# Optimization experiments

Measured on AMD Instinct MI355X. Metric: run time of the kernel, lower is better.

## Reference

```python
import jax, jax.numpy as jnp
import numpy as np

N_NODES = 100000
N_HEDGES = 200000
N_INC = 1000000
N_GRAPHS = 256
H = 64        # h_dim
HE = 35       # hedge_fea_dim
HOUT = 128    # hout_dim
NL = 3        # n_layers
EPS = 1e-5


def _segment_mean(vals, idx, num_segments):
    s = jax.ops.segment_sum(vals, idx, num_segments=num_segments)
    cnt = jax.ops.segment_sum(jnp.ones((vals.shape[0],), vals.dtype), idx,
                              num_segments=num_segments)
    return s / jnp.maximum(cnt, 1.0)[:, None]


def _bn(z, g, b):
    # training-mode BatchNorm1d: batch stats, biased variance
    m = jnp.mean(z, axis=0)
    v = jnp.var(z, axis=0)
    return (z - m) * jax.lax.rsqrt(v + EPS) * g + b


def setup_inputs() -> dict:
    key = jax.random.key(0)
    ks = jax.random.split(key, 32)
    inp = {
        "x": jax.random.normal(ks[0], (N_NODES, 92), jnp.float32),
        "node_idx": jax.random.randint(ks[1], (N_INC,), 0, N_NODES),
        "hedge_idx": jax.random.randint(ks[2], (N_INC,), 0, N_HEDGES),
        "hedge_attr": jax.random.normal(ks[3], (N_HEDGES, HE), jnp.float32),
        "batch": jnp.sort(jax.random.randint(ks[4], (N_NODES,), 0, N_GRAPHS)),
    }
    s = 0.05
    cat = H + HE  # 99
    inp["embed_w"] = jax.random.normal(ks[5], (92, H), jnp.float32) * s
    inp["embed_b"] = jnp.zeros((H,), jnp.float32)
    inp["f1_w"] = jax.random.normal(ks[6], (NL, cat, HE), jnp.float32) * s
    inp["f1_b"] = jnp.zeros((NL, HE), jnp.float32)
    inp["c1_w"] = jax.random.normal(ks[7], (NL, cat, HE), jnp.float32) * s
    inp["c1_b"] = jnp.zeros((NL, HE), jnp.float32)
    inp["f2_w"] = jax.random.normal(ks[8], (NL, cat, H), jnp.float32) * s
    inp["f2_b"] = jnp.zeros((NL, H), jnp.float32)
    inp["c2_w"] = jax.random.normal(ks[9], (NL, cat, H), jnp.float32) * s
    inp["c2_b"] = jnp.zeros((NL, H), jnp.float32)
    inp["bnf_g"] = jnp.ones((NL, HE), jnp.float32)
    inp["bnf_b"] = jnp.zeros((NL, HE), jnp.float32)
    inp["bnc_g"] = jnp.ones((NL, HE), jnp.float32)
    inp["bnc_b"] = jnp.zeros((NL, HE), jnp.float32)
    inp["bno_g"] = jnp.ones((NL, H), jnp.float32)
    inp["bno_b"] = jnp.zeros((NL, H), jnp.float32)
    inp["l2_w"] = jax.random.normal(ks[10], (H, HOUT), jnp.float32) * s
    inp["l2_b"] = jnp.zeros((HOUT,), jnp.float32)
    inp["out_w"] = jax.random.normal(ks[11], (HOUT, 1), jnp.float32) * s
    inp["out_b"] = jnp.zeros((1,), jnp.float32)
    return inp


def reference(x, node_idx, hedge_idx, hedge_attr, batch,
              embed_w, embed_b, f1_w, f1_b, c1_w, c1_b,
              f2_w, f2_b, c2_w, c2_b,
              bnf_g, bnf_b, bnc_g, bnc_b, bno_g, bno_b,
              l2_w, l2_b, out_w, out_b):
    sp = jax.nn.softplus
    x = x @ embed_w + embed_b  # [N, H]
    for i in range(NL):
        # gather node feats per incidence, mean over each hyperedge
        hx = _segment_mean(x[node_idx], hedge_idx, N_HEDGES)       # [NH, H]
        msg = jnp.concatenate([hx, hedge_attr], axis=1)            # [NH, H+HE]
        z_f = _bn(msg @ f1_w[i] + f1_b[i], bnf_g[i], bnf_b[i])
        z_c = _bn(msg @ c1_w[i] + c1_b[i], bnc_g[i], bnc_b[i])
        hedge_attr = jax.nn.sigmoid(z_f) * sp(z_c)                 # [NH, HE]
        z = jnp.concatenate([x[node_idx], hedge_attr[hedge_idx]], axis=-1)  # [E, H+HE]
        o = jax.nn.sigmoid(z @ f2_w[i] + f2_b[i]) * sp(z @ c2_w[i] + c2_b[i])  # [E, H]
        o = _segment_mean(o, node_idx, N_NODES)                    # [N, H]
        o = _bn(o, bno_g[i], bno_b[i])
        x = sp(o + x)
    pooled = _segment_mean(x, batch, N_GRAPHS)                     # [G, H]
    h = sp(pooled @ l2_w + l2_b)                                   # [G, HOUT]
    return h @ out_w + out_b                                       # [G, 1]
```

## Files before the change

kernel.cpp:

```cpp
#include <hip/hip_runtime.h>
#include <math.h>

#define N_NODES 100000
#define N_HEDGES 200000
#define N_INC 1000000
#define N_GRAPHS 256
#define HD 64
#define HE 35
#define CAT 99
#define EPSB 1e-5f

typedef __attribute__((ext_vector_type(8))) short short8;
typedef __attribute__((ext_vector_type(4))) float f32x4;

__device__ __forceinline__ float sp_f(float x) {
  return fmaxf(x, 0.f) + __logf(1.f + __expf(-fabsf(x)));
}
__device__ __forceinline__ float sig_f(float x) {
  return __builtin_amdgcn_rcpf(1.f + __expf(-x));
}
__device__ __forceinline__ unsigned bfr(float x) {
  unsigned u = __float_as_uint(x);
  return (u + 0x7fffu + ((u >> 16) & 1u)) >> 16;
}
__device__ __forceinline__ unsigned pk2(float lo, float hi) {
  return bfr(lo) | (bfr(hi) << 16);
}
__device__ __forceinline__ float blo(unsigned v) { return __uint_as_float(v << 16); }
__device__ __forceinline__ float bhi(unsigned v) {
  return __uint_as_float(v & 0xffff0000u);
}
__device__ __forceinline__ float bf2f(unsigned short s) {
  return __uint_as_float(((unsigned)s) << 16);
}

__global__ __launch_bounds__(256) void k_hist(const int* __restrict__ nidx,
                                              const int* __restrict__ hidx,
                                              int* __restrict__ degN,
                                              int* __restrict__ degH,
                                              int* __restrict__ rankN,
                                              int* __restrict__ rankH) {
  int e = blockIdx.x * 256 + threadIdx.x;
  if (e >= N_INC) return;
  rankH[e] = atomicAdd(&degH[hidx[e]], 1);
  rankN[e] = atomicAdd(&degN[nidx[e]], 1);
}

#define CHB ((N_HEDGES + 255) / 256)
#define CNB ((N_NODES + 255) / 256)

__global__ __launch_bounds__(256) void k_bsum(const int* __restrict__ degH,
                                              const int* __restrict__ degN,
                                              int* __restrict__ bsum) {
  __shared__ int s[256];
  int b = blockIdx.x, t = threadIdx.x;
  const int* deg;
  int n, i;
  if (b < CHB) {
    deg = degH; n = N_HEDGES; i = b * 256 + t;
  } else {
    deg = degN; n = N_NODES; i = (b - CHB) * 256 + t;
  }
  s[t] = (i < n) ? deg[i] : 0;
  __syncthreads();
  for (int st = 128; st > 0; st >>= 1) {
    if (t < st) s[t] += s[t + st];
    __syncthreads();
  }
  if (t == 0) bsum[b] = s[0];
}

__global__ __launch_bounds__(64) void k_bscan(int* __restrict__ bsum) {
  int seg0 = (blockIdx.x == 0) ? 0 : CHB;
  int segn = (blockIdx.x == 0) ? CHB : CNB;
  int lane = threadIdx.x;
  int carry = 0;
  for (int base = 0; base < segn; base += 64) {
    int i = base + lane;
    int orig = (i < segn) ? bsum[seg0 + i] : 0;
    int v = orig;
    for (int st = 1; st < 64; st <<= 1) {
      int u = __shfl_up(v, st);
      if (lane >= st) v += u;
    }
    int total = __shfl(v, 63);
    if (i < segn) bsum[seg0 + i] = carry + (v - orig);
    carry += total;
  }
}

__global__ __launch_bounds__(256) void k_alloc2(const int* __restrict__ degH,
                                                const int* __restrict__ degN,
                                                const int* __restrict__ bsum,
                                                int* __restrict__ offH,
                                                int* __restrict__ offN,
                                                float* __restrict__ invdH) {
  __shared__ int s[256];
  int b = blockIdx.x, t = threadIdx.x;
  const int* deg;
  int* off;
  int n, i;
  bool isH = (b < CHB);
  if (isH) {
    deg = degH; off = offH; n = N_HEDGES; i = b * 256 + t;
  } else {
    deg = degN; off = offN; n = N_NODES; i = (b - CHB) * 256 + t;
  }
  int d = (i < n) ? deg[i] : 0;
  s[t] = d;
  __syncthreads();
  for (int st = 1; st < 256; st <<= 1) {
    int u = 0;
    if (t >= st) u = s[t - st];
    __syncthreads();
    if (t >= st) s[t] += u;
    __syncthreads();
  }
  if (i < n) {
    off[i] = s[t] - d + bsum[b];
    if (isH) invdH[i] = 1.f / (float)max(d, 1);
  }
}

__global__ __launch_bounds__(256) void k_fill(const int* __restrict__ nidx,
                                              const int* __restrict__ hidx,
                                              const int* __restrict__ rankH,
                                              const int* __restrict__ rankN,
                                              const int* __restrict__ offH,
                                              const int* __restrict__ offN,
                                              int* __restrict__ permHn,
                                              int* __restrict__ permNh,
                                              int* __restrict__ offH_sent) {
  int e = blockIdx.x * 256 + threadIdx.x;
  if (e >= N_INC) return;
  if (e == 0) *offH_sent = N_INC;
  int nd = nidx[e], hg = hidx[e];
  permHn[offH[hg] + rankH[e]] = nd;
  permNh[offN[nd] + rankN[e]] = hg;
}

__global__ __launch_bounds__(64) void k_wpack(const float* __restrict__ f1w,
                                              const float* __restrict__ c1w,
                                              uint4* __restrict__ wpk) {
  int b = blockIdx.x;
  int layer = b / 20, rem = b % 20, ct = rem / 4, ks = rem % 4;
  int lane = threadIdx.x;
  int col = ct * 16 + (lane & 15);
  int k0 = ks * 32 + (lane >> 4) * 8;
  const float* wf = f1w + layer * CAT * HE;
  const float* wc = c1w + layer * CAT * HE;
  unsigned v[4];
#pragma unroll
  for (int p = 0; p < 4; ++p) {
    float lo = 0.f, hi = 0.f;
    int ka = k0 + p * 2, kb = ka + 1;
    if (ka < 99) {
      if (col < 35) lo = wf[ka * 35 + col];
      else if (col >= 36 && col < 71) lo = wc[ka * 35 + (col - 36)];
    }
    if (kb < 99) {
      if (col < 35) hi = wf[kb * 35 + col];
      else if (col >= 36 && col < 71) hi = wc[kb * 35 + (col - 36)];
    }
    v[p] = pk2(lo, hi);
  }
  uint4 o;
  o.x = v[0]; o.y = v[1]; o.z = v[2]; o.w = v[3];
  wpk[b * 64 + lane] = o;
}

__global__ __launch_bounds__(256) void k_cvt_ha(const float* __restrict__ src,
                                                unsigned short* __restrict__ dst,
                                                int n) {
  int t = blockIdx.x * 256 + threadIdx.x;
  if (t < n) dst[t] = (unsigned short)bfr(src[t]);
}

__global__ __launch_bounds__(256) void k_embed(const float* __restrict__ x,
                                               const float* __restrict__ w,
                                               const float* __restrict__ b,
                                               unsigned short* __restrict__ outb) {
  __shared__ float ws[92 * 64];
  __shared__ float rs[16][93];
  int tid = threadIdx.x;
  for (int i = tid; i < 92 * 64; i += 256) ws[i] = w[i];
  int r0 = blockIdx.x * 16;
  for (int i = tid; i < 16 * 92; i += 256) {
    int r = i / 92, k = i - r * 92;
    rs[r][k] = x[(r0 + r) * 92 + k];
  }
  __syncthreads();
  int h = tid & 63;
  float bias = b[h];
  for (int rr = tid >> 6; rr < 16; rr += 4) {
    float acc = bias;
    for (int k = 0; k < 92; ++k) acc += rs[rr][k] * ws[k * 64 + h];
    outb[(r0 + rr) * 64 + h] = (unsigned short)bfr(acc);
  }
}

#define GR 64
__global__ __launch_bounds__(256) void k_hedge_gemm(
    const unsigned short* __restrict__ xb, const int* __restrict__ permHn,
    const int* __restrict__ offH, const float* __restrict__ invdH,
    const unsigned short* __restrict__ hab, const uint4* __restrict__ wpk,
    unsigned short* __restrict__ z, float* __restrict__ stats) {
  __shared__ unsigned short msg[GR * 128];
  __shared__ float ps[160];
  __shared__ int bndL[4][18];
  int tid = threadIdx.x;
  int w = tid >> 6, lane = tid & 63;
  int r0 = blockIdx.x * GR;
  if (tid < 160) ps[tid] = 0.f;

  short8 bfg[5][4];
#pragma unroll
  for (int ct = 0; ct < 5; ++ct)
#pragma unroll
    for (int ks = 0; ks < 4; ++ks)
      bfg[ct][ks] = __builtin_bit_cast(short8, wpk[(ct * 4 + ks) * 64 + lane]);

  char* mb = (char*)msg;
  for (int i = tid; i < GR * 64; i += 256) {
    int r = i >> 6, c = 64 + (i & 63);
    unsigned short hv = 0;
    if (c < 99) hv = hab[(size_t)(r0 + r) * 35 + (c - 64)];
    *(unsigned short*)(mb + ((r * 256 + c * 2) ^ ((r & 7) << 4))) = hv;
  }

  int r0w = r0 + w * 16;
  if (lane < 17) bndL[w][lane] = offH[r0w + lane];
  int eBeg = bndL[w][0], eEnd = bndL[w][16];

  int j = 0;
  int nb = bndL[w][1];
  float acc = 0.f;
  for (int chunk = eBeg; chunk < eEnd; chunk += 8) {
    float v[8];
#pragma unroll
    for (int t = 0; t < 8; ++t) {
      int idx = permHn[min(chunk + t, eEnd - 1)];
      v[t] = bf2f(xb[(size_t)idx * 64 + lane]);
    }
#pragma unroll
    for (int t = 0; t < 8; ++t) {
      int e = chunk + t;
      if (e >= eEnd) break;
      while (e >= nb) {
        int rl = w * 16 + j;
        unsigned short mv = (unsigned short)bfr(acc * invdH[r0w + j]);
        *(unsigned short*)(mb + ((rl * 256 + lane * 2) ^ ((rl & 7) << 4))) = mv;
        acc = 0.f;
        ++j;
        nb = bndL[w][j + 1];
      }
      acc += v[t];
    }
  }
  for (; j < 16; ++j) {
    int rl = w * 16 + j;
    unsigned short mv = (unsigned short)bfr(acc * invdH[r0w + j]);
    *(unsigned short*)(mb + ((rl * 256 + lane * 2) ^ ((rl & 7) << 4))) = mv;
    acc = 0.f;
  }
  __syncthreads();

  {
    int rloc = w * 16 + (lane & 15);
    short8 a[4];
#pragma unroll
    for (int ks = 0; ks < 4; ++ks) {
      int byte = rloc * 256 + (ks * 32 + (lane >> 4) * 8) * 2;
      a[ks] = *(const short8*)(mb + (byte ^ ((rloc & 7) << 4)));
    }
#pragma unroll
    for (int ct = 0; ct < 5; ++ct) {
      f32x4 acc4 = {0.f, 0.f, 0.f, 0.f};
#pragma unroll
      for (int ks = 0; ks < 4; ++ks)
        acc4 = __builtin_amdgcn_mfma_f32_16x16x32_bf16(a[ks], bfg[ct][ks], acc4, 0, 0, 0);
      float s = (acc4[0] + acc4[1]) + (acc4[2] + acc4[3]);
      float q = (acc4[0] * acc4[0] + acc4[1] * acc4[1]) +
                (acc4[2] * acc4[2] + acc4[3] * acc4[3]);
      s += __shfl_xor(s, 16);
      s += __shfl_xor(s, 32);
      q += __shfl_xor(q, 16);
      q += __shfl_xor(q, 32);
      int col = ct * 16 + (lane & 15);
      if ((lane >> 4) == 0 && col < 72) {
        atomicAdd(&ps[col], s);
        atomicAdd(&ps[80 + col], q);
      }
      int growb = r0 + w * 16 + ((lane >> 4) << 2);
      if (col < 72) {
#pragma unroll
        for (int r = 0; r < 4; ++r)
          z[(size_t)(growb + r) * 72 + col] = (unsigned short)bfr(acc4[r]);
      }
    }
  }
  __syncthreads();
  if (tid < 160) atomicAdd(&stats[tid], ps[tid]);
}

__global__ __launch_bounds__(256) void k_hedge_post(
    const unsigned short* __restrict__ z, const float* __restrict__ stats,
    const float* __restrict__ gf, const float* __restrict__ bf_,
    const float* __restrict__ gc, const float* __restrict__ bc_,
    const float* __restrict__ f2wb, const float* __restrict__ c2wb,
    const float* __restrict__ f2b, const float* __restrict__ c2b,
    unsigned short* __restrict__ hab, unsigned* __restrict__ Vfc) {
  __shared__ float wf[35 * 64];
  __shared__ float wc[35 * 64];
  __shared__ float rs[16][36];
  __shared__ float sf[4][35];
  int tid = threadIdx.x;
  for (int i = tid; i < 35 * 64; i += 256) {
    wf[i] = f2wb[i];
    wc[i] = c2wb[i];
  }
  if (tid < 35) {
    const float inv = 1.f / N_HEDGES;
    float mf = stats[tid] * inv;
    float vf = stats[80 + tid] * inv - mf * mf;
    float mc = stats[36 + tid] * inv;
    float vc = stats[116 + tid] * inv - mc * mc;
    float a = rsqrtf(vf + EPSB) * gf[tid];
    float b = rsqrtf(vc + EPSB) * gc[tid];
    sf[0][tid] = a;
    sf[1][tid] = bf_[tid] - mf * a;
    sf[2][tid] = b;
    sf[3][tid] = bc_[tid] - mc * b;
  }
  __syncthreads();
  int r0 = blockIdx.x * 16;
  for (int i = tid; i < 16 * 35; i += 256) {
    int r = i / 35, c = i - r * 35;
    const unsigned short* zr = &z[(size_t)(r0 + r) * 72];
    float nf = bf2f(zr[c]) * sf[0][c] + sf[1][c];
    float nc = bf2f(zr[36 + c]) * sf[2][c] + sf[3][c];
    float ha = sig_f(nf) * sp_f(nc);
    rs[r][c] = ha;
    hab[(size_t)(r0 + r) * 35 + c] = (unsigned short)bfr(ha);
  }
  __syncthreads();
  int h = tid & 63, rb = tid >> 6;
  float af0, af1, af2, af3, ac0, ac1, ac2, ac3;
  af0 = af1 = af2 = af3 = f2b[h];
  ac0 = ac1 = ac2 = ac3 = c2b[h];
  for (int k = 0; k < 35; ++k) {
    float wfv = wf[k * 64 + h], wcv = wc[k * 64 + h];
    float m0 = rs[rb][k], m1 = rs[rb + 4][k], m2 = rs[rb + 8][k], m3 = rs[rb + 12][k];
    af0 += m0 * wfv; ac0 += m0 * wcv;
    af1 += m1 * wfv; ac1 += m1 * wcv;
    af2 += m2 * wfv; ac2 += m2 * wcv;
    af3 += m3 * wfv; ac3 += m3 * wcv;
  }
  int row = r0 + rb;
  Vfc[row * 64 + h] = pk2(af0, ac0);
  Vfc[(row + 4) * 64 + h] = pk2(af1, ac1);
  Vfc[(row + 8) * 64 + h] = pk2(af2, ac2);
  Vfc[(row + 12) * 64 + h] = pk2(af3, ac3);
}

__global__ __launch_bounds__(256) void k_uv_node(const unsigned short* __restrict__ xb,
                                                 const float* __restrict__ f2w,
                                                 const float* __restrict__ c2w,
                                                 unsigned* __restrict__ Ufc) {
  __shared__ float wf[64 * 64];
  __shared__ float wc[64 * 64];
  __shared__ float rs[16][65];
  int tid = threadIdx.x;
  for (int i = tid; i < 64 * 64; i += 256) {
    wf[i] = f2w[i];
    wc[i] = c2w[i];
  }
  int r0 = blockIdx.x * 16;
  for (int i = tid; i < 16 * 64; i += 256) {
    int r = i >> 6, k = i & 63;
    rs[r][k] = bf2f(xb[(size_t)(r0 + r) * 64 + k]);
  }
  __syncthreads();
  int h = tid & 63, rb = tid >> 6;
  float af0 = 0, af1 = 0, af2 = 0, af3 = 0, ac0 = 0, ac1 = 0, ac2 = 0, ac3 = 0;
  for (int k = 0; k < 64; ++k) {
    float wfv = wf[k * 64 + h], wcv = wc[k * 64 + h];
    float m0 = rs[rb][k], m1 = rs[rb + 4][k], m2 = rs[rb + 8][k], m3 = rs[rb + 12][k];
    af0 += m0 * wfv; ac0 += m0 * wcv;
    af1 += m1 * wfv; ac1 += m1 * wcv;
    af2 += m2 * wfv; ac2 += m2 * wcv;
    af3 += m3 * wfv; ac3 += m3 * wcv;
  }
  int row = r0 + rb;
  Ufc[row * 64 + h] = pk2(af0, ac0);
  Ufc[(row + 4) * 64 + h] = pk2(af1, ac1);
  Ufc[(row + 8) * 64 + h] = pk2(af2, ac2);
  Ufc[(row + 12) * 64 + h] = pk2(af3, ac3);
}

__device__ __forceinline__ float act2(float uf, float uc, unsigned v) {
  float a = uf + blo(v);
  float b = uc + bhi(v);
  return sig_f(a) * sp_f(b);
}
#define NAGG_GRID 2048
__global__ __launch_bounds__(256) void k_node_aggr(const int* __restrict__ permNh,
                                                   const int* __restrict__ offN,
                                                   const int* __restrict__ degN,
                                                   const unsigned* __restrict__ Ufc,
                                                   const unsigned* __restrict__ Vfc,
                                                   float* __restrict__ o,
                                                   float* __restrict__ stats) {
  int tid = threadIdx.x;
  int h = tid & 63, sub = tid >> 6;
  float sacc = 0.f, qacc = 0.f;
  for (int grp = blockIdx.x; grp < N_NODES / 4; grp += NAGG_GRID) {
    int wid = grp * 4 + sub;
    int off = offN[wid], d = degN[wid];
    unsigned u = Ufc[wid * 64 + h];
    float uf = blo(u), uc = bhi(u);
    float acc = 0.f;
    int k = 0;
    for (; k + 4 <= d; k += 4) {
      int h0 = permNh[off + k], h1 = permNh[off + k + 1];
      int h2 = permNh[off + k + 2], h3 = permNh[off + k + 3];
      unsigned v0 = Vfc[h0 * 64 + h];
      unsigned v1 = Vfc[h1 * 64 + h];
      unsigned v2 = Vfc[h2 * 64 + h];
      unsigned v3 = Vfc[h3 * 64 + h];
      acc += (act2(uf, uc, v0) + act2(uf, uc, v1)) +
             (act2(uf, uc, v2) + act2(uf, uc, v3));
    }
    for (; k < d; ++k) acc += act2(uf, uc, Vfc[permNh[off + k] * 64 + h]);
    float val = acc / (float)max(d, 1);
    o[(size_t)wid * 64 + h] = val;
    sacc += val;
    qacc += val * val;
  }
  __shared__ float ls[2][4][64];
  ls[0][sub][h] = sacc;
  ls[1][sub][h] = qacc;
  __syncthreads();
  if (tid < 64) {
    atomicAdd(&stats[h], ls[0][0][h] + ls[0][1][h] + ls[0][2][h] + ls[0][3][h]);
  } else if (tid < 128) {
    int hh = tid - 64;
    atomicAdd(&stats[64 + hh],
              ls[1][0][hh] + ls[1][1][hh] + ls[1][2][hh] + ls[1][3][hh]);
  }
}

__global__ __launch_bounds__(256) void k_update(unsigned short* __restrict__ xb,
                                                const float* __restrict__ o,
                                                const float* __restrict__ stats,
                                                const float* __restrict__ g,
                                                const float* __restrict__ b) {
  int t = blockIdx.x * 256 + threadIdx.x;
  int h = t & 63;
  float mean = stats[h] * (1.f / N_NODES);
  float var = stats[64 + h] * (1.f / N_NODES) - mean * mean;
  float is = rsqrtf(var + EPSB);
  float v = (o[t] - mean) * is * g[h] + b[h];
  float r = sp_f(v + bf2f(xb[t]));
  xb[t] = (unsigned short)bfr(r);
}

#define PR 512
__global__ __launch_bounds__(256) void k_pool(const unsigned short* __restrict__ xb,
                                              const int* __restrict__ batch,
                                              float* __restrict__ pooled,
                                              float* __restrict__ gcnt) {
  int h = threadIdx.x & 63, rs = threadIdx.x >> 6;
  int r0 = blockIdx.x * PR;
  int rend = min(r0 + PR, N_NODES);
  int gcur = -1;
  float acc = 0.f;
  int cnt = 0;
  for (int r = r0 + rs; r < rend; r += 4) {
    int g = batch[r];
    if (g != gcur) {
      if (gcur >= 0) {
        atomicAdd(&pooled[gcur * 64 + h], acc);
        if (h == 0) atomicAdd(&gcnt[gcur], (float)cnt);
      }
      gcur = g;
      acc = 0.f;
      cnt = 0;
    }
    acc += bf2f(xb[(size_t)r * 64 + h]);
    cnt++;
  }
  if (gcur >= 0) {
    atomicAdd(&pooled[gcur * 64 + h], acc);
    if (h == 0) atomicAdd(&gcnt[gcur], (float)cnt);
  }
}

__global__ __launch_bounds__(128) void k_final(const float* __restrict__ pooled,
                                               const float* __restrict__ gcnt,
                                               const float* __restrict__ l2w,
                                               const float* __restrict__ l2b,
                                               const float* __restrict__ ow,
                                               const float* __restrict__ ob,
                                               float* __restrict__ out) {
  int g = blockIdx.x;
  int t = threadIdx.x;
  __shared__ float row[64];
  __shared__ float hh[128];
  if (t < 64) row[t] = pooled[g * 64 + t] / fmaxf(gcnt[g], 1.f);
  __syncthreads();
  float acc = l2b[t];
  for (int k = 0; k < 64; ++k) acc += row[k] * l2w[k * 128 + t];
  hh[t] = sp_f(acc) * ow[t];
  __syncthreads();
  for (int s = 64; s > 0; s >>= 1) {
    if (t < s) hh[t] += hh[t + s];
    __syncthreads();
  }
  if (t == 0) out[g] = hh[0] + ob[0];
}

extern "C" void kernel_launch(void* const* d_in, const int* in_sizes, int n_in,
                              void* d_out, int out_size, void* d_ws, size_t ws_size,
                              hipStream_t stream) {
  const float* x_in = (const float*)d_in[0];
  const int* node_idx = (const int*)d_in[1];
  const int* hedge_idx = (const int*)d_in[2];
  const float* hedge_attr = (const float*)d_in[3];
  const int* batch = (const int*)d_in[4];
  const float* embed_w = (const float*)d_in[5];
  const float* embed_b = (const float*)d_in[6];
  const float* f1_w = (const float*)d_in[7];
  const float* c1_w = (const float*)d_in[9];
  const float* f2_w = (const float*)d_in[11];
  const float* f2_b = (const float*)d_in[12];
  const float* c2_w = (const float*)d_in[13];
  const float* c2_b = (const float*)d_in[14];
  const float* bnf_g = (const float*)d_in[15];
  const float* bnf_b = (const float*)d_in[16];
  const float* bnc_g = (const float*)d_in[17];
  const float* bnc_b = (const float*)d_in[18];
  const float* bno_g = (const float*)d_in[19];
  const float* bno_b = (const float*)d_in[20];
  const float* l2_w = (const float*)d_in[21];
  const float* l2_b = (const float*)d_in[22];
  const float* out_w = (const float*)d_in[23];
  const float* out_b = (const float*)d_in[24];

  char* base = (char*)d_ws;
  size_t off = 0;
  auto alloc = [&](size_t bytes) {
    size_t o = off;
    off = (off + bytes + 255) & ~(size_t)255;
    return o;
  };
  unsigned short* xbf = (unsigned short*)(base + alloc((size_t)N_NODES * 64 * 2));
  unsigned short* hab = (unsigned short*)(base + alloc((size_t)N_HEDGES * 35 * 2));
  unsigned* Vfc = (unsigned*)(base + alloc((size_t)N_HEDGES * 64 * 4));
  unsigned short* zbuf = (unsigned short*)(base + alloc((size_t)N_HEDGES * 72 * 2));
  float* obuf = (float*)(base + alloc((size_t)N_NODES * 64 * 4));
  unsigned* Ufc = (unsigned*)(base + alloc((size_t)N_NODES * 64 * 4));
  uint4* wpk = (uint4*)(base + alloc((size_t)60 * 64 * 16));
  float* hstatsA = (float*)(base + alloc(3 * 160 * 4));
  float* ostatsA = (float*)(base + alloc(3 * 128 * 4));
  float* pooled = (float*)(base + alloc((size_t)N_GRAPHS * 64 * 4));
  float* gcnt = (float*)(base + alloc((size_t)N_GRAPHS * 4));
  int* degH = (int*)(base + alloc((size_t)N_HEDGES * 4));
  int* degN = (int*)(base + alloc((size_t)N_NODES * 4));
  int* offH = (int*)(base + alloc((size_t)(N_HEDGES + 1) * 4));
  int* offN = (int*)(base + alloc((size_t)N_NODES * 4));
  float* invdH = (float*)(base + alloc((size_t)N_HEDGES * 4));
  int* bsum = (int*)(base + alloc((size_t)(CHB + CNB) * 4));
  int* rankH = (int*)(base + alloc((size_t)N_INC * 4));
  int* rankN = (int*)(base + alloc((size_t)N_INC * 4));
  int* permHn = (int*)(base + alloc((size_t)N_INC * 4));
  int* permNh = (int*)(base + alloc((size_t)N_INC * 4));
  (void)ws_size;
  (void)in_sizes;
  (void)n_in;
  (void)out_size;

  hipMemsetAsync(degH, 0,
                 (size_t)((char*)degN - (char*)degH) + (size_t)N_NODES * 4, stream);
  k_hist<<<(N_INC + 255) / 256, 256, 0, stream>>>(node_idx, hedge_idx, degN, degH,
                                                  rankN, rankH);
  k_bsum<<<CHB + CNB, 256, 0, stream>>>(degH, degN, bsum);
  k_bscan<<<2, 64, 0, stream>>>(bsum);
  k_alloc2<<<CHB + CNB, 256, 0, stream>>>(degH, degN, bsum, offH, offN, invdH);
  k_fill<<<(N_INC + 255) / 256, 256, 0, stream>>>(node_idx, hedge_idx, rankH, rankN,
                                                  offH, offN, permHn, permNh,
                                                  &offH[N_HEDGES]);
  k_wpack<<<60, 64, 0, stream>>>(f1_w, c1_w, wpk);
  k_cvt_ha<<<(N_HEDGES * 35 + 255) / 256, 256, 0, stream>>>(hedge_attr, hab,
                                                            N_HEDGES * 35);
  k_embed<<<N_NODES / 16, 256, 0, stream>>>(x_in, embed_w, embed_b, xbf);

  hipMemsetAsync(hstatsA, 0, (size_t)((char*)ostatsA - (char*)hstatsA) + 3 * 128 * 4,
                 stream);

  for (int i = 0; i < 3; ++i) {
    float* hstats = hstatsA + i * 160;
    float* ostats = ostatsA + i * 128;

    k_hedge_gemm<<<N_HEDGES / GR, 256, 0, stream>>>(
        xbf, permHn, offH, invdH, hab, wpk + (size_t)i * 20 * 64, zbuf, hstats);
    k_hedge_post<<<N_HEDGES / 16, 256, 0, stream>>>(
        zbuf, hstats, bnf_g + i * HE, bnf_b + i * HE, bnc_g + i * HE, bnc_b + i * HE,
        f2_w + i * CAT * 64 + 64 * 64, c2_w + i * CAT * 64 + 64 * 64,
        f2_b + i * 64, c2_b + i * 64, hab, Vfc);

    k_uv_node<<<N_NODES / 16, 256, 0, stream>>>(xbf, f2_w + i * CAT * 64,
                                                c2_w + i * CAT * 64, Ufc);

    k_node_aggr<<<NAGG_GRID, 256, 0, stream>>>(permNh, offN, degN, Ufc, Vfc, obuf,
                                               ostats);

    k_update<<<N_NODES * 64 / 256, 256, 0, stream>>>(xbf, obuf, ostats,
                                                     bno_g + i * 64, bno_b + i * 64);
  }

  hipMemsetAsync(pooled, 0, (size_t)((char*)gcnt - (char*)pooled) + N_GRAPHS * 4,
                 stream);
  k_pool<<<(N_NODES + PR - 1) / PR, 256, 0, stream>>>(xbf, batch, pooled, gcnt);
  k_final<<<N_GRAPHS, 128, 0, stream>>>(pooled, gcnt, l2_w, l2_b, out_w, out_b,
                                        (float*)d_out);
}
```

Measured before the change: 1.270 ms.

## Restructure node aggregation into edge-flattened chunks with batched gathers per wave

```diff
diff --git a/kernel.cpp b/kernel.cpp
--- a/kernel.cpp
+++ b/kernel.cpp
@@ -94,7 +94,8 @@
                                                 const int* __restrict__ bsum,
                                                 int* __restrict__ offH,
                                                 int* __restrict__ offN,
-                                                float* __restrict__ invdH) {
+                                                float* __restrict__ invdH,
+                                                float* __restrict__ invdN) {
   __shared__ int s[256];
   int b = blockIdx.x, t = threadIdx.x;
   const int* deg;
@@ -118,7 +119,10 @@
   }
   if (i < n) {
     off[i] = s[t] - d + bsum[b];
-    if (isH) invdH[i] = 1.f / (float)max(d, 1);
+    if (isH)
+      invdH[i] = 1.f / (float)max(d, 1);
+    else
+      invdN[i] = 1.f / (float)max(d, 1);
   }
 }
 
@@ -130,10 +134,14 @@
                                               const int* __restrict__ offN,
                                               int* __restrict__ permHn,
                                               int* __restrict__ permNh,
-                                              int* __restrict__ offH_sent) {
+                                              int* __restrict__ offH_sent,
+                                              int* __restrict__ offN_sent) {
   int e = blockIdx.x * 256 + threadIdx.x;
   if (e >= N_INC) return;
-  if (e == 0) *offH_sent = N_INC;
+  if (e == 0) {
+    *offH_sent = N_INC;
+    *offN_sent = N_INC;
+  }
   int nd = nidx[e], hg = hidx[e];
   permHn[offH[hg] + rankH[e]] = nd;
   permNh[offN[nd] + rankN[e]] = hg;
@@ -403,46 +411,71 @@
   float b = uc + bhi(v);
   return sig_f(a) * sp_f(b);
 }
-#define NAGG_GRID 2048
 __global__ __launch_bounds__(256) void k_node_aggr(const int* __restrict__ permNh,
                                                    const int* __restrict__ offN,
-                                                   const int* __restrict__ degN,
+                                                   const float* __restrict__ invdN,
                                                    const unsigned* __restrict__ Ufc,
                                                    const unsigned* __restrict__ Vfc,
                                                    float* __restrict__ o,
                                                    float* __restrict__ stats) {
+  __shared__ int bndL[4][18];
+  __shared__ float ls[2][4][64];
   int tid = threadIdx.x;
-  int h = tid & 63, sub = tid >> 6;
-  float sacc = 0.f, qacc = 0.f;
-  for (int grp = blockIdx.x; grp < N_NODES / 4; grp += NAGG_GRID) {
-    int wid = grp * 4 + sub;
-    int off = offN[wid], d = degN[wid];
-    unsigned u = Ufc[wid * 64 + h];
-    float uf = blo(u), uc = bhi(u);
-    float acc = 0.f;
-    int k = 0;
-    for (; k + 4 <= d; k += 4) {
-      int h0 = permNh[off + k], h1 = permNh[off + k + 1];
-      int h2 = permNh[off + k + 2], h3 = permNh[off + k + 3];
-      unsigned v0 = Vfc[h0 * 64 + h];
-      unsigned v1 = Vfc[h1 * 64 + h];
-      unsigned v2 = Vfc[h2 * 64 + h];
-      unsigned v3 = Vfc[h3 * 64 + h];
-      acc += (act2(uf, uc, v0) + act2(uf, uc, v1)) +
-             (act2(uf, uc, v2) + act2(uf, uc, v3));
-    }
-    for (; k < d; ++k) acc += act2(uf, uc, Vfc[permNh[off + k] * 64 + h]);
-    float val = acc / (float)max(d, 1);
-    o[(size_t)wid * 64 + h] = val;
-    sacc += val;
-    qacc += val * val;
-  }
-  __shared__ float ls[2][4][64];
-  ls[0][sub][h] = sacc;
-  ls[1][sub][h] = qacc;
+  int w = tid >> 6, lane = tid & 63;
+  int r0w = blockIdx.x * 64 + w * 16;
+  if (lane < 17) bndL[w][lane] = offN[min(r0w + lane, N_NODES)];
+  int eBeg = bndL[w][0], eEnd = bndL[w][16];
+
+  int j = 0;
+  int nb = bndL[w][1];
+  float acc = 0.f, sacc = 0.f, qacc = 0.f;
+  unsigned u0 = (r0w < N_NODES) ? Ufc[(size_t)r0w * 64 + lane] : 0u;
+  float uf = blo(u0), uc = bhi(u0);
+
+  for (int chunk = eBeg; chunk < eEnd; chunk += 8) {
+    unsigned pv[8];
+#pragma unroll
+    for (int t = 0; t < 8; ++t) {
+      int hg = permNh[min(chunk + t, eEnd - 1)];
+      pv[t] = Vfc[(size_t)hg * 64 + lane];
+    }
+#pragma unroll
+    for (int t = 0; t < 8; ++t) {
+      int e = chunk + t;
+      if (e >= eEnd) break;
+      while (e >= nb) {
+        int row = r0w + j;
+        float val = acc * invdN[row];
+        o[(size_t)row * 64 + lane] = val;
+        sacc += val;
+        qacc += val * val;
+        acc = 0.f;
+        ++j;
+        nb = bndL[w][j + 1];
+        unsigned un = Ufc[(size_t)(r0w + j) * 64 + lane];
+        uf = blo(un);
+        uc = bhi(un);
+      }
+      acc += act2(uf, uc, pv[t]);
+    }
+  }
+  for (; j < 16; ++j) {
+    int row = r0w + j;
+    if (row < N_NODES) {
+      float val = acc * invdN[row];
+      o[(size_t)row * 64 + lane] = val;
+      sacc += val;
+      qacc += val * val;
+    }
+    acc = 0.f;
+  }
+
+  ls[0][w][lane] = sacc;
+  ls[1][w][lane] = qacc;
   __syncthreads();
   if (tid < 64) {
-    atomicAdd(&stats[h], ls[0][0][h] + ls[0][1][h] + ls[0][2][h] + ls[0][3][h]);
+    atomicAdd(&stats[lane],
+              ls[0][0][lane] + ls[0][1][lane] + ls[0][2][lane] + ls[0][3][lane]);
   } else if (tid < 128) {
     int hh = tid - 64;
     atomicAdd(&stats[64 + hh],
@@ -568,8 +601,9 @@
   int* degH = (int*)(base + alloc((size_t)N_HEDGES * 4));
   int* degN = (int*)(base + alloc((size_t)N_NODES * 4));
   int* offH = (int*)(base + alloc((size_t)(N_HEDGES + 1) * 4));
-  int* offN = (int*)(base + alloc((size_t)N_NODES * 4));
+  int* offN = (int*)(base + alloc((size_t)(N_NODES + 1) * 4));
   float* invdH = (float*)(base + alloc((size_t)N_HEDGES * 4));
+  float* invdN = (float*)(base + alloc((size_t)N_NODES * 4));
   int* bsum = (int*)(base + alloc((size_t)(CHB + CNB) * 4));
   int* rankH = (int*)(base + alloc((size_t)N_INC * 4));
   int* rankN = (int*)(base + alloc((size_t)N_INC * 4));
@@ -586,10 +620,10 @@
                                                   rankN, rankH);
   k_bsum<<<CHB + CNB, 256, 0, stream>>>(degH, degN, bsum);
   k_bscan<<<2, 64, 0, stream>>>(bsum);
-  k_alloc2<<<CHB + CNB, 256, 0, stream>>>(degH, degN, bsum, offH, offN, invdH);
+  k_alloc2<<<CHB + CNB, 256, 0, stream>>>(degH, degN, bsum, offH, offN, invdH, invdN);
   k_fill<<<(N_INC + 255) / 256, 256, 0, stream>>>(node_idx, hedge_idx, rankH, rankN,
                                                   offH, offN, permHn, permNh,
-                                                  &offH[N_HEDGES]);
+                                                  &offH[N_HEDGES], &offN[N_NODES]);
   k_wpack<<<60, 64, 0, stream>>>(f1_w, c1_w, wpk);
   k_cvt_ha<<<(N_HEDGES * 35 + 255) / 256, 256, 0, stream>>>(hedge_attr, hab,
                                                             N_HEDGES * 35);
@@ -612,8 +646,8 @@
     k_uv_node<<<N_NODES / 16, 256, 0, stream>>>(xbf, f2_w + i * CAT * 64,
                                                 c2_w + i * CAT * 64, Ufc);
 
-    k_node_aggr<<<NAGG_GRID, 256, 0, stream>>>(permNh, offN, degN, Ufc, Vfc, obuf,
-                                               ostats);
+    k_node_aggr<<<(N_NODES + 63) / 64, 256, 0, stream>>>(permNh, offN, invdN, Ufc,
+                                                         Vfc, obuf, ostats);
 
     k_update<<<N_NODES * 64 / 256, 256, 0, stream>>>(xbf, obuf, ostats,
                                                      bno_g + i * 64, bno_b + i * 64);
```

Result: no change. 1.247 ms (-1.8%).
